# Optimization experiments

Hardware: AMD Instinct MI355X
Metric: run time of the kernel (lower is better)

Reference implementation:

```python
import jax, jax.numpy as jnp
from jax import lax
import numpy as np

BETA = 1.0


def setup_inputs() -> dict:
    key = jax.random.key(0)
    k1, k2, k3, k4, k5, k6 = jax.random.split(key, 6)
    B, S, D = 16, 2048, 768
    encoder_outputs = jax.random.normal(k1, (B, S, D), dtype=jnp.float32)
    encoder_lens = jax.random.randint(k2, (B,), 1, S + 1, dtype=jnp.int32)
    # AlphaNetwork params: Conv1d(D, D, kernel=3, padding same) + Linear(D, 1)
    conv_w = jax.random.normal(k3, (D, D, 3), dtype=jnp.float32) * (1.0 / np.sqrt(3 * D))
    conv_b = jax.random.normal(k4, (D,), dtype=jnp.float32) * 0.01
    lin_w = jax.random.normal(k5, (1, D), dtype=jnp.float32) * (1.0 / np.sqrt(D))
    lin_b = jax.random.normal(k6, (1,), dtype=jnp.float32) * 0.01
    return {"encoder_outputs": encoder_outputs, "encoder_lens": encoder_lens,
            "conv_w": conv_w, "conv_b": conv_b, "lin_w": lin_w, "lin_b": lin_b}


def _alpha_network(x, conv_w, conv_b, lin_w, lin_b):
    # x: (B, S, D) -> alphas (B, S)
    x_ncw = jnp.transpose(x, (0, 2, 1))  # (B, D, S)
    y = lax.conv_general_dilated(x_ncw, conv_w, window_strides=(1,), padding="SAME",
                                 dimension_numbers=("NCH", "OIH", "NCH"))
    y = y + conv_b[None, :, None]
    y = jnp.transpose(y, (0, 2, 1))  # (B, S, D)
    return jax.nn.sigmoid(jnp.einsum("bsd,od->bso", y, lin_w) + lin_b)[..., 0]


def _cif_single(h, alpha, length, beta=BETA):
    # h: (S, D), alpha: (S,), length: scalar int
    S, D = h.shape

    def step(carry, inputs):
        aacc, hacc = carry
        a_u, h_u, t = inputs
        valid = t < length
        aacc_u = aacc + a_u
        fire = (aacc_u >= beta) & valid
        a1 = 1.0 - aacc               # weight assigned to h_u for the emitted segment
        c = hacc + a1 * h_u           # emitted vector on fire
        a2 = a_u - a1                 # leftover weight carried to next segment
        new_aacc = jnp.where(fire, a2, jnp.where(valid, aacc_u, aacc))
        new_hacc = jnp.where(fire, a2 * h_u, jnp.where(valid, hacc + a_u * h_u, hacc))
        return (new_aacc, new_hacc), (fire, jnp.where(fire, c, jnp.zeros_like(c)))

    init = (jnp.zeros((), h.dtype), jnp.zeros((D,), h.dtype))
    _, (fired, cs) = lax.scan(step, init, (alpha, h, jnp.arange(S)))
    # compact fired vectors to the front; non-fired rows scatter to dropped bucket S
    pos = jnp.cumsum(fired.astype(jnp.int32)) - 1
    idx = jnp.where(fired, pos, S)
    out = jnp.zeros((S + 1, D), h.dtype).at[idx].set(cs)[:S]
    return out, jnp.sum(fired.astype(jnp.int32))


def reference(encoder_outputs, encoder_lens, conv_w, conv_b, lin_w, lin_b):
    alphas = _alpha_network(encoder_outputs, conv_w, conv_b, lin_w, lin_b)  # (B, S)
    output_c, len_tensor = jax.vmap(_cif_single)(encoder_outputs, alphas, encoder_lens)
    # output_c padded to seq_len (static upper bound on number of fires)
    return output_c, len_tensor
```

## Files before the change

kernel.cpp:

```cpp
#include <hip/hip_runtime.h>
#include <math.h>

#define BB 16
#define SS 2048
#define DD 768
#define NROW (BB * SS)
#define NSLICE 16

#define PART_OFF  0
#define W3_OFF    (PART_OFF + NSLICE*2304)
#define BIAS_OFF  (W3_OFF + 2304)
#define E0_OFF    (BIAS_OFF + 64)
#define E1_OFF    (E0_OFF + NROW)
#define E2_OFF    (E1_OFF + NROW)
#define WCUR_OFF  (E2_OFF + NROW)
#define WNEXT_OFF (WCUR_OFF + NROW)
#define FT_OFF    (WNEXT_OFF + NROW)
#define LEN_OFF   (FT_OFF + NROW)

__global__ __launch_bounds__(256) void k1a_fold_part(
    const float* __restrict__ conv_w, const float* __restrict__ lin_w,
    float* __restrict__ ws) {
  int tid = threadIdx.x;
  int slice = blockIdx.x / 9, cb = blockIdx.x % 9;
  int c = cb * 256 + tid;
  int o0 = slice * (DD / NSLICE);
  float acc = 0.f;
#pragma unroll 4
  for (int oo = 0; oo < DD / NSLICE; ++oo) {
    int o = o0 + oo;
    acc = fmaf(lin_w[o], conv_w[(size_t)o * 2304 + c], acc);
  }
  ws[PART_OFF + slice * 2304 + c] = acc;
}

__global__ __launch_bounds__(256) void k1r_fold_reduce(
    const float* __restrict__ conv_b, const float* __restrict__ lin_w,
    const float* __restrict__ lin_b, float* __restrict__ ws) {
  __shared__ float red[256];
  int tid = threadIdx.x;
  if (blockIdx.x < 9) {
    int c = blockIdx.x * 256 + tid;
    float acc = 0.f;
#pragma unroll
    for (int s = 0; s < NSLICE; ++s) acc += ws[PART_OFF + s * 2304 + c];
    int i = c / 3, k = c % 3;
    ws[W3_OFF + k * DD + i] = acc;
  } else {
    float p = 0.f;
    for (int o = tid; o < DD; o += 256) p = fmaf(lin_w[o], conv_b[o], p);
    red[tid] = p;
    __syncthreads();
    for (int off = 128; off > 0; off >>= 1) {
      if (tid < off) red[tid] += red[tid + off];
      __syncthreads();
    }
    if (tid == 0) ws[BIAS_OFF] = red[0] + lin_b[0];
  }
}

__global__ __launch_bounds__(256) void k2a_dots(
    const float* __restrict__ x, const float* __restrict__ ws,
    float* __restrict__ e0, float* __restrict__ e1, float* __restrict__ e2) {
  __shared__ float w3[2304];
  int tid = threadIdx.x;
  for (int c = tid; c < 2304; c += 256) w3[c] = ws[W3_OFF + c];
  __syncthreads();
  int wave = tid >> 6, lane = tid & 63;
  int row = blockIdx.x * 4 + wave;
  const float4* xr = (const float4*)(x + (size_t)row * DD);
  const float4* w0p = (const float4*)(w3);
  const float4* w1p = (const float4*)(w3 + DD);
  const float4* w2p = (const float4*)(w3 + 2 * DD);
  float a0 = 0.f, a1 = 0.f, a2 = 0.f;
#pragma unroll
  for (int q = 0; q < 3; ++q) {
    int f = lane + q * 64;
    float4 xv = xr[f];
    float4 w0 = w0p[f], w1 = w1p[f], w2 = w2p[f];
    a0 += w0.x * xv.x + w0.y * xv.y + w0.z * xv.z + w0.w * xv.w;
    a1 += w1.x * xv.x + w1.y * xv.y + w1.z * xv.z + w1.w * xv.w;
    a2 += w2.x * xv.x + w2.y * xv.y + w2.z * xv.z + w2.w * xv.w;
  }
#pragma unroll
  for (int m = 1; m < 64; m <<= 1) {
    a0 += __shfl_xor(a0, m);
    a1 += __shfl_xor(a1, m);
    a2 += __shfl_xor(a2, m);
  }
  if (lane == 0) { e0[row] = a0; e1[row] = a1; e2[row] = a2; }
}

__global__ __launch_bounds__(256) void k3_scan(
    const float* __restrict__ ws_ro, const int* __restrict__ lens,
    float* __restrict__ wcur, float* __restrict__ wnext, int* __restrict__ ft,
    int* __restrict__ lenws, float* __restrict__ out_len) {
  __shared__ double sscan[256];
  int b = blockIdx.x, tid = threadIdx.x;
  const float* e0 = ws_ro + E0_OFF + b * SS;
  const float* e1 = ws_ro + E1_OFF + b * SS;
  const float* e2 = ws_ro + E2_OFF + b * SS;
  float bias = ws_ro[BIAS_OFF];
  int len = lens[b];
  int t0 = tid * 8;
  float a[8];
  double incl[8];
  double run = 0.0;
#pragma unroll
  for (int e = 0; e < 8; ++e) {
    int t = t0 + e;
    float z = bias + e1[t];
    if (t > 0) z += e0[t - 1];
    if (t < SS - 1) z += e2[t + 1];
    float av = 1.f / (1.f + expf(-z));
    a[e] = (t < len) ? av : 0.f;
    run += (double)a[e];
    incl[e] = run;
  }
  sscan[tid] = run;
  __syncthreads();
  for (int off = 1; off < 256; off <<= 1) {
    double v = (tid >= off) ? sscan[tid - off] : 0.0;
    __syncthreads();
    sscan[tid] += v;
    __syncthreads();
  }
  double excl = (tid == 0) ? 0.0 : sscan[tid - 1];
  double Pprev = excl;
  int Fprev = (int)floor(excl);
#pragma unroll
  for (int e = 0; e < 8; ++e) {
    int t = t0 + e;
    double P = excl + incl[e];
    int F = (int)floor(P);
    bool fire = (F > Fprev);
    float wc = fire ? (float)((double)F - Pprev) : a[e];
    float wn = fire ? (float)(P - (double)F) : 0.f;
    wcur[b * SS + t] = wc;
    wnext[b * SS + t] = wn;
    if (fire) ft[b * SS + (F - 1)] = t;
    Pprev = P;
    Fprev = F;
  }
  if (tid == 0) {
    int L = (int)floor(sscan[255]);
    lenws[b] = L;
    out_len[b] = (float)L;
  }
}

__global__ __launch_bounds__(256) void k4_emit(
    const float* __restrict__ x, const float* __restrict__ wcur,
    const float* __restrict__ wnext, const int* __restrict__ ft,
    const int* __restrict__ lenws, float* __restrict__ out) {
  int tid = threadIdx.x, wave = tid >> 6, lane = tid & 63;
  int row = blockIdx.x * 4 + wave;
  int b = row >> 11, j = row & (SS - 1);
  float4* orow = (float4*)(out + (size_t)row * DD);
  int L = lenws[b];
  if (j >= L) {
    float4 z = {0.f, 0.f, 0.f, 0.f};
    orow[lane] = z;
    orow[lane + 64] = z;
    orow[lane + 128] = z;
    return;
  }
  int start = (j == 0) ? 0 : ft[b * SS + j - 1];
  int end = ft[b * SS + j];
  float4 acc0 = {0, 0, 0, 0}, acc1 = {0, 0, 0, 0}, acc2 = {0, 0, 0, 0};
  for (int t = start; t <= end; ++t) {
    float w = (j > 0 && t == start) ? wnext[b * SS + t] : wcur[b * SS + t];
    const float4* xr = (const float4*)(x + ((size_t)b * SS + t) * DD);
    float4 v0 = xr[lane], v1 = xr[lane + 64], v2 = xr[lane + 128];
    acc0.x = fmaf(w, v0.x, acc0.x); acc0.y = fmaf(w, v0.y, acc0.y);
    acc0.z = fmaf(w, v0.z, acc0.z); acc0.w = fmaf(w, v0.w, acc0.w);
    acc1.x = fmaf(w, v1.x, acc1.x); acc1.y = fmaf(w, v1.y, acc1.y);
    acc1.z = fmaf(w, v1.z, acc1.z); acc1.w = fmaf(w, v1.w, acc1.w);
    acc2.x = fmaf(w, v2.x, acc2.x); acc2.y = fmaf(w, v2.y, acc2.y);
    acc2.z = fmaf(w, v2.z, acc2.z); acc2.w = fmaf(w, v2.w, acc2.w);
  }
  orow[lane] = acc0;
  orow[lane + 64] = acc1;
  orow[lane + 128] = acc2;
}

extern "C" void kernel_launch(void* const* d_in, const int* in_sizes, int n_in,
                              void* d_out, int out_size, void* d_ws, size_t ws_size,
                              hipStream_t stream) {
  const float* x      = (const float*)d_in[0];
  const int*   lens   = (const int*)d_in[1];
  const float* conv_w = (const float*)d_in[2];
  const float* conv_b = (const float*)d_in[3];
  const float* lin_w  = (const float*)d_in[4];
  const float* lin_b  = (const float*)d_in[5];
  float* out = (float*)d_out;
  float* ws = (float*)d_ws;

  float* e0 = ws + E0_OFF;
  float* e1 = ws + E1_OFF;
  float* e2 = ws + E2_OFF;
  float* wc = ws + WCUR_OFF;
  float* wn = ws + WNEXT_OFF;
  int* ft = (int*)(ws + FT_OFF);
  int* lenws = (int*)(ws + LEN_OFF);
  float* out_len = out + (size_t)NROW * DD;

  k1a_fold_part<<<NSLICE * 9, 256, 0, stream>>>(conv_w, lin_w, ws);
  k1r_fold_reduce<<<10, 256, 0, stream>>>(conv_b, lin_w, lin_b, ws);
  k2a_dots<<<NROW / 4, 256, 0, stream>>>(x, ws, e0, e1, e2);
  k3_scan<<<BB, 256, 0, stream>>>(ws, lens, wc, wn, ft, lenws, out_len);
  k4_emit<<<NROW / 4, 256, 0, stream>>>(x, wc, wn, ft, lenws, out);
}
```

Baseline: 213.5 us.

## Fuse all stages into one cooperative persistent kernel with grid syncs

Replaces the five separate kernel launches with a single cooperative kernel of 1024 blocks that runs the weight fold, reduction, per-row dot products, scan and emit phases, separated by grid.sync(). Each block now handles 32 rows per phase in a loop instead of one block per 4 rows. This is meant to remove launch overhead and inter-kernel gaps. In exchange it adds four grid-wide barriers, and during the scan phase only 16 blocks do work while the rest of the grid idles at the barrier.

New measurement: 662.4 us. 210% more time.

```diff
diff --git a/kernel.cpp b/kernel.cpp
--- a/kernel.cpp
+++ b/kernel.cpp
@@ -1,10 +1,14 @@
 #include <hip/hip_runtime.h>
+#include <hip/hip_cooperative_groups.h>
 #include <math.h>
+
+namespace cg = cooperative_groups;
 
 #define BB 16
 #define SS 2048
 #define DD 768
 #define NROW (BB * SS)
+#define NBLK 1024
 #define NSLICE 16
 
 #define PART_OFF  0
@@ -18,35 +22,42 @@
 #define FT_OFF    (WNEXT_OFF + NROW)
 #define LEN_OFF   (FT_OFF + NROW)
 
-__global__ __launch_bounds__(256) void k1a_fold_part(
-    const float* __restrict__ conv_w, const float* __restrict__ lin_w,
-    float* __restrict__ ws) {
-  int tid = threadIdx.x;
-  int slice = blockIdx.x / 9, cb = blockIdx.x % 9;
-  int c = cb * 256 + tid;
-  int o0 = slice * (DD / NSLICE);
-  float acc = 0.f;
+__global__ __launch_bounds__(256, 4) void cif_mega(
+    const float* __restrict__ x, const int* __restrict__ lens,
+    const float* __restrict__ conv_w, const float* __restrict__ conv_b,
+    const float* __restrict__ lin_w, const float* __restrict__ lin_b,
+    float* __restrict__ ws, float* __restrict__ out) {
+  cg::grid_group grid = cg::this_grid();
+  __shared__ float w3s[2304];
+  __shared__ double sscan[256];
+
+  const int tid = threadIdx.x;
+  const int blk = blockIdx.x;
+  const int wave = tid >> 6, lane = tid & 63;
+
+  if (blk < NSLICE * 9) {
+    int slice = blk / 9, cb = blk % 9;
+    int c = cb * 256 + tid;
+    int o0 = slice * (DD / NSLICE);
+    float acc = 0.f;
 #pragma unroll 4
-  for (int oo = 0; oo < DD / NSLICE; ++oo) {
-    int o = o0 + oo;
-    acc = fmaf(lin_w[o], conv_w[(size_t)o * 2304 + c], acc);
-  }
-  ws[PART_OFF + slice * 2304 + c] = acc;
-}
-
-__global__ __launch_bounds__(256) void k1r_fold_reduce(
-    const float* __restrict__ conv_b, const float* __restrict__ lin_w,
-    const float* __restrict__ lin_b, float* __restrict__ ws) {
-  __shared__ float red[256];
-  int tid = threadIdx.x;
-  if (blockIdx.x < 9) {
-    int c = blockIdx.x * 256 + tid;
+    for (int oo = 0; oo < DD / NSLICE; ++oo) {
+      int o = o0 + oo;
+      acc = fmaf(lin_w[o], conv_w[(size_t)o * 2304 + c], acc);
+    }
+    ws[PART_OFF + slice * 2304 + c] = acc;
+  }
+  grid.sync();
+
+  if (blk < 9) {
+    int c = blk * 256 + tid;
     float acc = 0.f;
 #pragma unroll
     for (int s = 0; s < NSLICE; ++s) acc += ws[PART_OFF + s * 2304 + c];
     int i = c / 3, k = c % 3;
     ws[W3_OFF + k * DD + i] = acc;
-  } else {
+  } else if (blk == 9) {
+    __shared__ float red[256];
     float p = 0.f;
     for (int o = tid; o < DD; o += 256) p = fmaf(lin_w[o], conv_b[o], p);
     red[tid] = p;
@@ -57,131 +68,139 @@
     }
     if (tid == 0) ws[BIAS_OFF] = red[0] + lin_b[0];
   }
-}
-
-__global__ __launch_bounds__(256) void k2a_dots(
-    const float* __restrict__ x, const float* __restrict__ ws,
-    float* __restrict__ e0, float* __restrict__ e1, float* __restrict__ e2) {
-  __shared__ float w3[2304];
-  int tid = threadIdx.x;
-  for (int c = tid; c < 2304; c += 256) w3[c] = ws[W3_OFF + c];
+  grid.sync();
+
+  for (int c = tid; c < 2304; c += 256) w3s[c] = ws[W3_OFF + c];
   __syncthreads();
-  int wave = tid >> 6, lane = tid & 63;
-  int row = blockIdx.x * 4 + wave;
-  const float4* xr = (const float4*)(x + (size_t)row * DD);
-  const float4* w0p = (const float4*)(w3);
-  const float4* w1p = (const float4*)(w3 + DD);
-  const float4* w2p = (const float4*)(w3 + 2 * DD);
-  float a0 = 0.f, a1 = 0.f, a2 = 0.f;
-#pragma unroll
-  for (int q = 0; q < 3; ++q) {
-    int f = lane + q * 64;
-    float4 xv = xr[f];
-    float4 w0 = w0p[f], w1 = w1p[f], w2 = w2p[f];
-    a0 += w0.x * xv.x + w0.y * xv.y + w0.z * xv.z + w0.w * xv.w;
-    a1 += w1.x * xv.x + w1.y * xv.y + w1.z * xv.z + w1.w * xv.w;
-    a2 += w2.x * xv.x + w2.y * xv.y + w2.z * xv.z + w2.w * xv.w;
-  }
-#pragma unroll
-  for (int m = 1; m < 64; m <<= 1) {
-    a0 += __shfl_xor(a0, m);
-    a1 += __shfl_xor(a1, m);
-    a2 += __shfl_xor(a2, m);
-  }
-  if (lane == 0) { e0[row] = a0; e1[row] = a1; e2[row] = a2; }
-}
-
-__global__ __launch_bounds__(256) void k3_scan(
-    const float* __restrict__ ws_ro, const int* __restrict__ lens,
-    float* __restrict__ wcur, float* __restrict__ wnext, int* __restrict__ ft,
-    int* __restrict__ lenws, float* __restrict__ out_len) {
-  __shared__ double sscan[256];
-  int b = blockIdx.x, tid = threadIdx.x;
-  const float* e0 = ws_ro + E0_OFF + b * SS;
-  const float* e1 = ws_ro + E1_OFF + b * SS;
-  const float* e2 = ws_ro + E2_OFF + b * SS;
-  float bias = ws_ro[BIAS_OFF];
-  int len = lens[b];
-  int t0 = tid * 8;
-  float a[8];
-  double incl[8];
-  double run = 0.0;
-#pragma unroll
-  for (int e = 0; e < 8; ++e) {
-    int t = t0 + e;
-    float z = bias + e1[t];
-    if (t > 0) z += e0[t - 1];
-    if (t < SS - 1) z += e2[t + 1];
-    float av = 1.f / (1.f + expf(-z));
-    a[e] = (t < len) ? av : 0.f;
-    run += (double)a[e];
-    incl[e] = run;
-  }
-  sscan[tid] = run;
-  __syncthreads();
-  for (int off = 1; off < 256; off <<= 1) {
-    double v = (tid >= off) ? sscan[tid - off] : 0.0;
+  {
+    const float4* w0p = (const float4*)(w3s);
+    const float4* w1p = (const float4*)(w3s + DD);
+    const float4* w2p = (const float4*)(w3s + 2 * DD);
+    float* e0 = ws + E0_OFF;
+    float* e1 = ws + E1_OFF;
+    float* e2 = ws + E2_OFF;
+    int base = blk * 32;
+#pragma unroll 2
+    for (int it = 0; it < 8; ++it) {
+      int row = base + it * 4 + wave;
+      const float4* xr = (const float4*)(x + (size_t)row * DD);
+      float a0 = 0.f, a1 = 0.f, a2 = 0.f;
+#pragma unroll
+      for (int q = 0; q < 3; ++q) {
+        int f = lane + q * 64;
+        float4 xv = xr[f];
+        float4 w0 = w0p[f], w1 = w1p[f], w2 = w2p[f];
+        a0 += w0.x * xv.x + w0.y * xv.y + w0.z * xv.z + w0.w * xv.w;
+        a1 += w1.x * xv.x + w1.y * xv.y + w1.z * xv.z + w1.w * xv.w;
+        a2 += w2.x * xv.x + w2.y * xv.y + w2.z * xv.z + w2.w * xv.w;
+      }
+#pragma unroll
+      for (int m = 1; m < 64; m <<= 1) {
+        a0 += __shfl_xor(a0, m);
+        a1 += __shfl_xor(a1, m);
+        a2 += __shfl_xor(a2, m);
+      }
+      if (lane == 0) { e0[row] = a0; e1[row] = a1; e2[row] = a2; }
+    }
+  }
+  grid.sync();
+
+  if (blk < BB) {
+    int b = blk;
+    const float* e0 = ws + E0_OFF + b * SS;
+    const float* e1 = ws + E1_OFF + b * SS;
+    const float* e2 = ws + E2_OFF + b * SS;
+    float* wcur = ws + WCUR_OFF;
+    float* wnext = ws + WNEXT_OFF;
+    int* ft = (int*)(ws + FT_OFF);
+    int* lenws = (int*)(ws + LEN_OFF);
+    float bias = ws[BIAS_OFF];
+    int len = lens[b];
+    int t0 = tid * 8;
+    float a[8];
+    double incl[8];
+    double run = 0.0;
+#pragma unroll
+    for (int e = 0; e < 8; ++e) {
+      int t = t0 + e;
+      float z = bias + e1[t];
+      if (t > 0) z += e0[t - 1];
+      if (t < SS - 1) z += e2[t + 1];
+      float av = 1.f / (1.f + expf(-z));
+      a[e] = (t < len) ? av : 0.f;
+      run += (double)a[e];
+      incl[e] = run;
+    }
+    sscan[tid] = run;
     __syncthreads();
-    sscan[tid] += v;
-    __syncthreads();
-  }
-  double excl = (tid == 0) ? 0.0 : sscan[tid - 1];
-  double Pprev = excl;
-  int Fprev = (int)floor(excl);
-#pragma unroll
-  for (int e = 0; e < 8; ++e) {
-    int t = t0 + e;
-    double P = excl + incl[e];
-    int F = (int)floor(P);
-    bool fire = (F > Fprev);
-    float wc = fire ? (float)((double)F - Pprev) : a[e];
-    float wn = fire ? (float)(P - (double)F) : 0.f;
-    wcur[b * SS + t] = wc;
-    wnext[b * SS + t] = wn;
-    if (fire) ft[b * SS + (F - 1)] = t;
-    Pprev = P;
-    Fprev = F;
-  }
-  if (tid == 0) {
-    int L = (int)floor(sscan[255]);
-    lenws[b] = L;
-    out_len[b] = (float)L;
-  }
-}
-
-__global__ __launch_bounds__(256) void k4_emit(
-    const float* __restrict__ x, const float* __restrict__ wcur,
-    const float* __restrict__ wnext, const int* __restrict__ ft,
-    const int* __restrict__ lenws, float* __restrict__ out) {
-  int tid = threadIdx.x, wave = tid >> 6, lane = tid & 63;
-  int row = blockIdx.x * 4 + wave;
-  int b = row >> 11, j = row & (SS - 1);
-  float4* orow = (float4*)(out + (size_t)row * DD);
-  int L = lenws[b];
-  if (j >= L) {
-    float4 z = {0.f, 0.f, 0.f, 0.f};
-    orow[lane] = z;
-    orow[lane + 64] = z;
-    orow[lane + 128] = z;
-    return;
-  }
-  int start = (j == 0) ? 0 : ft[b * SS + j - 1];
-  int end = ft[b * SS + j];
-  float4 acc0 = {0, 0, 0, 0}, acc1 = {0, 0, 0, 0}, acc2 = {0, 0, 0, 0};
-  for (int t = start; t <= end; ++t) {
-    float w = (j > 0 && t == start) ? wnext[b * SS + t] : wcur[b * SS + t];
-    const float4* xr = (const float4*)(x + ((size_t)b * SS + t) * DD);
-    float4 v0 = xr[lane], v1 = xr[lane + 64], v2 = xr[lane + 128];
-    acc0.x = fmaf(w, v0.x, acc0.x); acc0.y = fmaf(w, v0.y, acc0.y);
-    acc0.z = fmaf(w, v0.z, acc0.z); acc0.w = fmaf(w, v0.w, acc0.w);
-    acc1.x = fmaf(w, v1.x, acc1.x); acc1.y = fmaf(w, v1.y, acc1.y);
-    acc1.z = fmaf(w, v1.z, acc1.z); acc1.w = fmaf(w, v1.w, acc1.w);
-    acc2.x = fmaf(w, v2.x, acc2.x); acc2.y = fmaf(w, v2.y, acc2.y);
-    acc2.z = fmaf(w, v2.z, acc2.z); acc2.w = fmaf(w, v2.w, acc2.w);
-  }
-  orow[lane] = acc0;
-  orow[lane + 64] = acc1;
-  orow[lane + 128] = acc2;
+    for (int off = 1; off < 256; off <<= 1) {
+      double v = (tid >= off) ? sscan[tid - off] : 0.0;
+      __syncthreads();
+      sscan[tid] += v;
+      __syncthreads();
+    }
+    double excl = (tid == 0) ? 0.0 : sscan[tid - 1];
+    double Pprev = excl;
+    int Fprev = (int)floor(excl);
+#pragma unroll
+    for (int e = 0; e < 8; ++e) {
+      int t = t0 + e;
+      double P = excl + incl[e];
+      int F = (int)floor(P);
+      bool fire = (F > Fprev);
+      float wc = fire ? (float)((double)F - Pprev) : a[e];
+      float wn = fire ? (float)(P - (double)F) : 0.f;
+      wcur[b * SS + t] = wc;
+      wnext[b * SS + t] = wn;
+      if (fire) ft[b * SS + (F - 1)] = t;
+      Pprev = P;
+      Fprev = F;
+    }
+    if (tid == 0) {
+      int L = (int)floor(sscan[255]);
+      lenws[b] = L;
+      out[(size_t)NROW * DD + b] = (float)L;
+    }
+  }
+  grid.sync();
+
+  {
+    const float* wcur = ws + WCUR_OFF;
+    const float* wnext = ws + WNEXT_OFF;
+    const int* ft = (const int*)(ws + FT_OFF);
+    const int* lenws = (const int*)(ws + LEN_OFF);
+    int base = blk * 32;
+    for (int it = 0; it < 8; ++it) {
+      int row = base + it * 4 + wave;
+      int b = row >> 11, j = row & (SS - 1);
+      float4* orow = (float4*)(out + (size_t)row * DD);
+      int L = lenws[b];
+      if (j >= L) {
+        float4 z = {0.f, 0.f, 0.f, 0.f};
+        orow[lane] = z;
+        orow[lane + 64] = z;
+        orow[lane + 128] = z;
+        continue;
+      }
+      int start = (j == 0) ? 0 : ft[b * SS + j - 1];
+      int end = ft[b * SS + j];
+      float4 acc0 = {0, 0, 0, 0}, acc1 = {0, 0, 0, 0}, acc2 = {0, 0, 0, 0};
+      for (int t = start; t <= end; ++t) {
+        float w = (j > 0 && t == start) ? wnext[b * SS + t] : wcur[b * SS + t];
+        const float4* xr = (const float4*)(x + ((size_t)b * SS + t) * DD);
+        float4 v0 = xr[lane], v1 = xr[lane + 64], v2 = xr[lane + 128];
+        acc0.x = fmaf(w, v0.x, acc0.x); acc0.y = fmaf(w, v0.y, acc0.y);
+        acc0.z = fmaf(w, v0.z, acc0.z); acc0.w = fmaf(w, v0.w, acc0.w);
+        acc1.x = fmaf(w, v1.x, acc1.x); acc1.y = fmaf(w, v1.y, acc1.y);
+        acc1.z = fmaf(w, v1.z, acc1.z); acc1.w = fmaf(w, v1.w, acc1.w);
+        acc2.x = fmaf(w, v2.x, acc2.x); acc2.y = fmaf(w, v2.y, acc2.y);
+        acc2.z = fmaf(w, v2.z, acc2.z); acc2.w = fmaf(w, v2.w, acc2.w);
+      }
+      orow[lane] = acc0;
+      orow[lane + 64] = acc1;
+      orow[lane + 128] = acc2;
+    }
+  }
 }
 
 extern "C" void kernel_launch(void* const* d_in, const int* in_sizes, int n_in,
@@ -196,18 +215,10 @@
   float* out = (float*)d_out;
   float* ws = (float*)d_ws;
 
-  float* e0 = ws + E0_OFF;
-  float* e1 = ws + E1_OFF;
-  float* e2 = ws + E2_OFF;
-  float* wc = ws + WCUR_OFF;
-  float* wn = ws + WNEXT_OFF;
-  int* ft = (int*)(ws + FT_OFF);
-  int* lenws = (int*)(ws + LEN_OFF);
-  float* out_len = out + (size_t)NROW * DD;
-
-  k1a_fold_part<<<NSLICE * 9, 256, 0, stream>>>(conv_w, lin_w, ws);
-  k1r_fold_reduce<<<10, 256, 0, stream>>>(conv_b, lin_w, lin_b, ws);
-  k2a_dots<<<NROW / 4, 256, 0, stream>>>(x, ws, e0, e1, e2);
-  k3_scan<<<BB, 256, 0, stream>>>(ws, lens, wc, wn, ft, lenws, out_len);
-  k4_emit<<<NROW / 4, 256, 0, stream>>>(x, wc, wn, ft, lenws, out);
+  void* kargs[] = {
+    (void*)&x, (void*)&lens, (void*)&conv_w, (void*)&conv_b,
+    (void*)&lin_w, (void*)&lin_b, (void*)&ws, (void*)&out,
+  };
+  hipLaunchCooperativeKernel(reinterpret_cast<void*>(cif_mega),
+                             dim3(NBLK), dim3(256), kargs, 0u, stream);
 }
```

## Skip dot products past sequence length and use wave-shuffle scan

Applied to the files above, without the earlier changes.

The per-row dot-product kernel now reads each batch's length and exits early for rows beyond it, so it no longer reads x for padded timesteps. The scan kernel also computes the sigmoid only for valid timesteps. Its shared-memory Hillis-Steele prefix sum over 256 doubles is replaced by a 64-lane shuffle scan plus a small cross-wave offset. Skipped rows leave e0/e1/e2 unwritten, which is safe only because the scan reads them solely for t < len (and t+1 <= len).

Result: faster. 202.4 us (-5.2%).

```diff
diff --git a/kernel.cpp b/kernel.cpp
--- a/kernel.cpp
+++ b/kernel.cpp
@@ -61,13 +61,17 @@
 
 __global__ __launch_bounds__(256) void k2a_dots(
     const float* __restrict__ x, const float* __restrict__ ws,
+    const int* __restrict__ lens,
     float* __restrict__ e0, float* __restrict__ e1, float* __restrict__ e2) {
   __shared__ float w3[2304];
   int tid = threadIdx.x;
+  int wave = tid >> 6, lane = tid & 63;
+  int row = blockIdx.x * 4 + wave;
+  int b = row >> 11, s = row & (SS - 1);
+  bool active = (s <= lens[b]);
   for (int c = tid; c < 2304; c += 256) w3[c] = ws[W3_OFF + c];
   __syncthreads();
-  int wave = tid >> 6, lane = tid & 63;
-  int row = blockIdx.x * 4 + wave;
+  if (!active) return;
   const float4* xr = (const float4*)(x + (size_t)row * DD);
   const float4* w0p = (const float4*)(w3);
   const float4* w1p = (const float4*)(w3 + DD);
@@ -95,8 +99,9 @@
     const float* __restrict__ ws_ro, const int* __restrict__ lens,
     float* __restrict__ wcur, float* __restrict__ wnext, int* __restrict__ ft,
     int* __restrict__ lenws, float* __restrict__ out_len) {
-  __shared__ double sscan[256];
+  __shared__ double wtot[4];
   int b = blockIdx.x, tid = threadIdx.x;
+  int wave = tid >> 6, lane = tid & 63;
   const float* e0 = ws_ro + E0_OFF + b * SS;
   const float* e1 = ws_ro + E1_OFF + b * SS;
   const float* e2 = ws_ro + E2_OFF + b * SS;
@@ -109,23 +114,28 @@
 #pragma unroll
   for (int e = 0; e < 8; ++e) {
     int t = t0 + e;
-    float z = bias + e1[t];
-    if (t > 0) z += e0[t - 1];
-    if (t < SS - 1) z += e2[t + 1];
-    float av = 1.f / (1.f + expf(-z));
-    a[e] = (t < len) ? av : 0.f;
-    run += (double)a[e];
+    float av = 0.f;
+    if (t < len) {
+      float z = bias + e1[t];
+      if (t > 0) z += e0[t - 1];
+      z += e2[t + 1];
+      av = 1.f / (1.f + expf(-z));
+    }
+    a[e] = av;
+    run += (double)av;
     incl[e] = run;
   }
-  sscan[tid] = run;
+  double v = run;
+#pragma unroll
+  for (int m = 1; m < 64; m <<= 1) {
+    double o = __shfl_up(v, m);
+    if (lane >= m) v += o;
+  }
+  if (lane == 63) wtot[wave] = v;
   __syncthreads();
-  for (int off = 1; off < 256; off <<= 1) {
-    double v = (tid >= off) ? sscan[tid - off] : 0.0;
-    __syncthreads();
-    sscan[tid] += v;
-    __syncthreads();
-  }
-  double excl = (tid == 0) ? 0.0 : sscan[tid - 1];
+  double woff = 0.0;
+  for (int w = 0; w < wave; ++w) woff += wtot[w];
+  double excl = woff + v - run;
   double Pprev = excl;
   int Fprev = (int)floor(excl);
 #pragma unroll
@@ -142,8 +152,8 @@
     Pprev = P;
     Fprev = F;
   }
-  if (tid == 0) {
-    int L = (int)floor(sscan[255]);
+  if (tid == 255) {
+    int L = (int)floor(woff + v);
     lenws[b] = L;
     out_len[b] = (float)L;
   }
@@ -207,7 +217,7 @@
 
   k1a_fold_part<<<NSLICE * 9, 256, 0, stream>>>(conv_w, lin_w, ws);
   k1r_fold_reduce<<<10, 256, 0, stream>>>(conv_b, lin_w, lin_b, ws);
-  k2a_dots<<<NROW / 4, 256, 0, stream>>>(x, ws, e0, e1, e2);
+  k2a_dots<<<NROW / 4, 256, 0, stream>>>(x, ws, lens, e0, e1, e2);
   k3_scan<<<BB, 256, 0, stream>>>(ws, lens, wc, wn, ft, lenws, out_len);
   k4_emit<<<NROW / 4, 256, 0, stream>>>(x, wc, wn, ft, lenws, out);
 }
```
